# Optimization experiments

Measured on AMD Instinct MI355X. Metric: run time of the kernel, lower is better.

## Reference

```python
import jax, jax.numpy as jnp
import numpy as np

EMBED_DIM = 1024
N1 = 4096
N2 = 4096


def setup_inputs() -> dict:
    key = jax.random.key(0)
    ks = jax.random.split(key, 14)
    s = 1.0 / np.sqrt(EMBED_DIM)
    def lin(k):
        kw, kb = jax.random.split(k)
        W = jax.random.uniform(kw, (EMBED_DIM, EMBED_DIM), jnp.float32, -s, s)
        b = jax.random.uniform(kb, (EMBED_DIM,), jnp.float32, -s, s)
        return W, b
    Wq1, bq1 = lin(ks[0]); Wk1, bk1 = lin(ks[1]); Wv1, bv1 = lin(ks[2])
    Wq2, bq2 = lin(ks[3]); Wk2, bk2 = lin(ks[4]); Wv2, bv2 = lin(ks[5])
    x1 = jax.random.normal(ks[6], (N1, EMBED_DIM), jnp.float32)
    x2 = jax.random.normal(ks[7], (N2, EMBED_DIM), jnp.float32)
    return {
        "input_tensor1": x1, "input_tensor2": x2,
        "Wq1": Wq1, "bq1": bq1, "Wk1": Wk1, "bk1": bk1, "Wv1": Wv1, "bv1": bv1,
        "Wq2": Wq2, "bq2": bq2, "Wk2": Wk2, "bk2": bk2, "Wv2": Wv2, "bv2": bv2,
    }


def reference(input_tensor1, input_tensor2,
              Wq1, bq1, Wk1, bk1, Wv1, bv1,
              Wq2, bq2, Wk2, bk2, Wv2, bv2):
    scale = 1.0 / jnp.sqrt(jnp.asarray(EMBED_DIM, input_tensor1.dtype))
    # torch Linear: y = x @ W.T + b
    q1 = input_tensor1 @ Wq1.T + bq1   # [N1, D]
    k1 = input_tensor1 @ Wk1.T + bk1
    v1 = input_tensor1 @ Wv1.T + bv1
    q2 = input_tensor2 @ Wq2.T + bq2   # [N2, D]
    k2 = input_tensor2 @ Wk2.T + bk2
    v2 = input_tensor2 @ Wv2.T + bv2
    # stream-2 queries attend over stream-1 keys/values
    scores1 = (q2 @ k1.T) * scale                  # [N2, N1]
    probs1 = jax.nn.softmax(scores1, axis=-1)      # dropout p=0 -> identity
    context1 = probs1 @ v1                         # [N2, D]
    # stream-1 queries attend over stream-2 keys/values
    scores2 = (q1 @ k2.T) * scale                  # [N1, N2]
    probs2 = jax.nn.softmax(scores2, axis=-1)
    context2 = probs2 @ v2                         # [N1, D]
    return (context1, context2)
```

## Files before the change

### kernel.cpp

```cpp
#include <hip/hip_runtime.h>
#include <hip/hip_bf16.h>
#include <cstdint>
#include <cstddef>

#define DEVINL __device__ __forceinline__

typedef __attribute__((ext_vector_type(4))) float   f32x4;
typedef __bf16 bf16x8 __attribute__((ext_vector_type(8)));
typedef __attribute__((ext_vector_type(4))) short   short4v;
typedef __attribute__((ext_vector_type(4))) float   float4v;

static constexpr int DIM = 1024;
static constexpr int NTOK = 4096;

DEVINL unsigned short f2bf(float f) {
  unsigned u = __float_as_uint(f);
  u += 0x7FFF + ((u >> 16) & 1);
  return (unsigned short)(u >> 16);
}
DEVINL float bf2f(unsigned short s) {
  return __uint_as_float(((unsigned)s) << 16);
}

DEVINL void gll16(const void* g, void* l) {
  __builtin_amdgcn_global_load_lds(
      (const __attribute__((address_space(1))) void*)g,
      (__attribute__((address_space(3))) void*)l, 16, 0, 0);
}

struct B3 { int bx, by, bz; };
DEVINL B3 xcd_remap(int GX, int GY, int GZ) {
  const int flat = blockIdx.x + GX * (blockIdx.y + GY * blockIdx.z);
  const int nwg  = GX * GY * GZ;
  const int chunk = nwg >> 3;
  const int vbid = (flat & 7) * chunk + (flat >> 3);
  B3 r;
  r.bx = vbid % GX;
  r.by = (vbid / GX) % GY;
  r.bz = vbid / (GX * GY);
  return r;
}

DEVINL void core128(const unsigned short* __restrict__ A, int lda,
                    const unsigned short* __restrict__ B, int ldb,
                    int K, int brow, int bcol, f32x4 acc[4][4])
{
  __shared__ unsigned short lds[32768];
  const int t = threadIdx.x;
  const int w = t >> 6, l = t & 63;
  const int wr = w >> 1, wc = w & 1;
  const int srow = (w << 3) + (l >> 3);
  const int scol = ((l & 7) ^ (l >> 3)) << 3;
  const int l15 = l & 15;
  const int cs0 = (((l >> 4) << 3)        ^ ((l & 7) << 3));
  const int cs1 = ((32 + ((l >> 4) << 3)) ^ ((l & 7) << 3));

  const unsigned short* aL = A + (size_t)(brow * 128 + srow) * lda + scol;
  const unsigned short* bL = B + (size_t)(bcol * 128 + srow) * ldb + scol;

#pragma unroll
  for (int m = 0; m < 4; ++m)
#pragma unroll
    for (int n = 0; n < 4; ++n) {
      f32x4 z = {0.f, 0.f, 0.f, 0.f};
      acc[m][n] = z;
    }

#define STAGE(buf, kt)                                                         \
  _Pragma("unroll")                                                            \
  for (int r = 0; r < 4; ++r) {                                                \
    gll16(aL + (size_t)(r * 32) * lda + (size_t)(kt) * 64,                     \
          lds + (buf) * 16384 + (r * 32 + (w << 3)) * 64);                     \
    gll16(bL + (size_t)(r * 32) * ldb + (size_t)(kt) * 64,                     \
          lds + (buf) * 16384 + 8192 + (r * 32 + (w << 3)) * 64);              \
  }

#define BARR() do { asm volatile("" ::: "memory");                             \
                    __builtin_amdgcn_s_barrier();                              \
                    asm volatile("" ::: "memory"); } while (0)

  const int NT = K >> 6;

  STAGE(0, 0);
  asm volatile("s_waitcnt vmcnt(0)" ::: "memory");
  BARR();

  bf16x8 af[4][2], bfv[4][2];
  for (int kt = 0; kt < NT; ++kt) {
    const int cur = kt & 1;
    if (kt + 1 < NT) STAGE(cur ^ 1, kt + 1);

#pragma unroll
    for (int m = 0; m < 4; ++m) {
      const unsigned short* p = lds + cur * 16384 + (wr * 64 + m * 16 + l15) * 64;
      af[m][0] = *(const bf16x8*)(p + cs0);
      af[m][1] = *(const bf16x8*)(p + cs1);
    }
#pragma unroll
    for (int n = 0; n < 4; ++n) {
      const unsigned short* p = lds + cur * 16384 + 8192 + (wc * 64 + n * 16 + l15) * 64;
      bfv[n][0] = *(const bf16x8*)(p + cs0);
      bfv[n][1] = *(const bf16x8*)(p + cs1);
    }

    __builtin_amdgcn_s_setprio(1);
#pragma unroll
    for (int m = 0; m < 4; ++m)
#pragma unroll
      for (int n = 0; n < 4; ++n) {
        f32x4 c_ = acc[m][n];
        c_ = __builtin_amdgcn_mfma_f32_16x16x32_bf16(af[m][0], bfv[n][0], c_, 0, 0, 0);
        c_ = __builtin_amdgcn_mfma_f32_16x16x32_bf16(af[m][1], bfv[n][1], c_, 0, 0, 0);
        acc[m][n] = c_;
      }
    __builtin_amdgcn_s_setprio(0);

    asm volatile("s_waitcnt vmcnt(0)" ::: "memory");
    BARR();
  }
#undef STAGE
#undef BARR
}

__global__ __launch_bounds__(256, 2)
void gemm128_scores(const unsigned short* __restrict__ A,
                    const unsigned short* __restrict__ B,
                    unsigned short* __restrict__ S, float scale)
{
  const B3 b = xcd_remap(32, 32, 1);
  f32x4 acc[4][4];
  core128(A, DIM, B, DIM, DIM, b.by, b.bx, acc);

  const int t = threadIdx.x, w = t >> 6, l = t & 63;
  const int wr = w >> 1, wc = w & 1;
  const int rr = (l >> 4) * 4, cc = l & 15;
#pragma unroll
  for (int m = 0; m < 4; ++m) {
    const int row0 = b.by * 128 + wr * 64 + m * 16 + rr;
#pragma unroll
    for (int n = 0; n < 4; ++n) {
      const int col = b.bx * 128 + wc * 64 + n * 16 + cc;
#pragma unroll
      for (int i = 0; i < 4; ++i)
        S[(size_t)(row0 + i) * NTOK + col] = f2bf(acc[m][n][i] * scale);
    }
  }
}

__global__ __launch_bounds__(256, 2)
void qkv128(const unsigned short* __restrict__ x1, const unsigned short* __restrict__ x2,
            const unsigned short* __restrict__ W6,
            const float* bq1, const float* bk1, const float* bv1,
            const float* bq2, const float* bk2, const float* bv2,
            unsigned short* q1, unsigned short* k1, unsigned short* v1T,
            unsigned short* q2, unsigned short* k2, unsigned short* v2T)
{
  const B3 b = xcd_remap(8, 32, 6);
  const int g = b.bz;
  const unsigned short* A = (g < 3) ? x1 : x2;
  const unsigned short* W = W6 + (size_t)g * (DIM * DIM);
  const float* bias = (g == 0) ? bq1 : (g == 1) ? bk1 : (g == 2) ? bv1
                    : (g == 3) ? bq2 : (g == 4) ? bk2 : bv2;
  unsigned short* out = (g == 0) ? q1 : (g == 1) ? k1 : (g == 2) ? v1T
                      : (g == 3) ? q2 : (g == 4) ? k2 : v2T;
  const bool vT = (g == 2 || g == 5);

  f32x4 acc[4][4];
  core128(A, DIM, W, DIM, DIM, b.by, b.bx, acc);

  const int t = threadIdx.x, w = t >> 6, l = t & 63;
  const int wr = w >> 1, wc = w & 1;
  const int rr = (l >> 4) * 4, cc = l & 15;

  if (!vT) {
#pragma unroll
    for (int m = 0; m < 4; ++m) {
      const int row0 = b.by * 128 + wr * 64 + m * 16 + rr;
#pragma unroll
      for (int n = 0; n < 4; ++n) {
        const int col = b.bx * 128 + wc * 64 + n * 16 + cc;
        const float bv_ = bias[col];
#pragma unroll
        for (int i = 0; i < 4; ++i)
          out[(size_t)(row0 + i) * DIM + col] = f2bf(acc[m][n][i] + bv_);
      }
    }
  } else {
#pragma unroll
    for (int m = 0; m < 4; ++m) {
      const int row0 = b.by * 128 + wr * 64 + m * 16 + rr;
#pragma unroll
      for (int n = 0; n < 4; ++n) {
        const int col = b.bx * 128 + wc * 64 + n * 16 + cc;
        const float bv_ = bias[col];
        short4v pk;
#pragma unroll
        for (int i = 0; i < 4; ++i) pk[i] = (short)f2bf(acc[m][n][i] + bv_);
        *(short4v*)(out + (size_t)col * NTOK + row0) = pk;
      }
    }
  }
}

__global__ __launch_bounds__(256, 2)
void pv128(const unsigned short* __restrict__ S1,
           const unsigned short* __restrict__ S2,
           const unsigned short* __restrict__ vTcat,
           float* __restrict__ out, float* __restrict__ P)
{
  const B3 b = xcd_remap(16, 32, 2);
  const int bx = b.bx, by = b.by, z = b.bz;
  const unsigned short* A = ((bx < 8) ? S1 : S2) + (size_t)z * 2048;
  const unsigned short* B = vTcat + (size_t)z * 2048;

  f32x4 acc[4][4];
  core128(A, NTOK, B, NTOK, 2048, by, bx, acc);

  const int t = threadIdx.x, w = t >> 6, l = t & 63;
  const int wr = w >> 1, wc = w & 1;
  const int rr = (l >> 4) * 4, cc = l & 15;
#pragma unroll
  for (int m = 0; m < 4; ++m) {
    const int row0 = by * 128 + wr * 64 + m * 16 + rr;
#pragma unroll
    for (int n = 0; n < 4; ++n) {
      const int cg = bx * 128 + wc * 64 + n * 16 + cc;
#pragma unroll
      for (int i = 0; i < 4; ++i) {
        const int r = row0 + i;
        if (z) {
          P[(size_t)r * 2048 + cg] = acc[m][n][i];
        } else {
          float* dst = (cg < 1024) ? (out + (size_t)r * 1024 + cg)
                                   : (out + 4194304 + (size_t)r * 1024 + (cg - 1024));
          *dst = acc[m][n][i];
        }
      }
    }
  }
}

__global__ __launch_bounds__(256)
void add_pv(float* __restrict__ out, const float* __restrict__ P)
{
  const int idx = blockIdx.x * 256 + threadIdx.x;
  const int r  = idx >> 9;
  const int c4 = (idx & 511) << 2;
  const float4v p = *(const float4v*)(P + (size_t)r * 2048 + c4);
  float* dst = (c4 < 1024) ? (out + (size_t)r * 1024 + c4)
                           : (out + 4194304 + (size_t)r * 1024 + (c4 - 1024));
  float4v a = *(const float4v*)dst;
#pragma unroll
  for (int j = 0; j < 4; ++j) a[j] += p[j];
  *(float4v*)dst = a;
}

__global__ __launch_bounds__(256)
void softmax_inplace(unsigned short* __restrict__ S)
{
  const int row = blockIdx.x;
  unsigned short* r = S + (size_t)row * NTOK;
  const int t = threadIdx.x, wave = t >> 6, lane = t & 63;
  __shared__ float red[4];

  bf16x8 d0 = *(const bf16x8*)(r + t * 8);
  bf16x8 d1 = *(const bf16x8*)(r + 2048 + t * 8);
  float v[16];
  {
    const unsigned short* p0 = (const unsigned short*)&d0;
    const unsigned short* p1 = (const unsigned short*)&d1;
#pragma unroll
    for (int j = 0; j < 8; ++j) { v[j] = bf2f(p0[j]); v[8 + j] = bf2f(p1[j]); }
  }
  float mx = v[0];
#pragma unroll
  for (int j = 1; j < 16; ++j) mx = fmaxf(mx, v[j]);
#pragma unroll
  for (int o = 32; o > 0; o >>= 1) mx = fmaxf(mx, __shfl_xor(mx, o));
  if (lane == 0) red[wave] = mx;
  __syncthreads();
  mx = fmaxf(fmaxf(red[0], red[1]), fmaxf(red[2], red[3]));

  float s = 0.f;
#pragma unroll
  for (int j = 0; j < 16; ++j) { v[j] = __expf(v[j] - mx); s += v[j]; }
#pragma unroll
  for (int o = 32; o > 0; o >>= 1) s += __shfl_xor(s, o);
  __syncthreads();
  if (lane == 0) red[wave] = s;
  __syncthreads();
  s = red[0] + red[1] + red[2] + red[3];
  const float inv = 1.0f / s;

  unsigned short o0[8], o1[8];
#pragma unroll
  for (int j = 0; j < 8; ++j) { o0[j] = f2bf(v[j] * inv); o1[j] = f2bf(v[8 + j] * inv); }
  *(bf16x8*)(r + t * 8)        = *(const bf16x8*)o0;
  *(bf16x8*)(r + 2048 + t * 8) = *(const bf16x8*)o1;
}

__global__ __launch_bounds__(256)
void cvt2(const float* __restrict__ a, const float* __restrict__ b,
          unsigned short* __restrict__ oa, unsigned short* __restrict__ ob)
{
  const float* in = blockIdx.y ? b : a;
  unsigned short* out = blockIdx.y ? ob : oa;
  const size_t i = ((size_t)blockIdx.x * 256 + threadIdx.x) * 4;
  float4v x = *(const float4v*)(in + i);
  short4v o;
#pragma unroll
  for (int j = 0; j < 4; ++j) o[j] = (short)f2bf(x[j]);
  *(short4v*)(out + i) = o;
}

__global__ __launch_bounds__(256)
void cvt_w(const float* w0, const float* w1, const float* w2,
           const float* w3, const float* w4, const float* w5,
           unsigned short* __restrict__ W6)
{
  const float* srcs[6] = {w0, w1, w2, w3, w4, w5};
  const float* in = srcs[blockIdx.y];
  unsigned short* out = W6 + (size_t)blockIdx.y * (DIM * DIM);
  const size_t i = ((size_t)blockIdx.x * 256 + threadIdx.x) * 4;
  float4v x = *(const float4v*)(in + i);
  short4v o;
#pragma unroll
  for (int j = 0; j < 4; ++j) o[j] = (short)f2bf(x[j]);
  *(short4v*)(out + i) = o;
}

extern "C" void kernel_launch(void* const* d_in, const int* in_sizes, int n_in,
                              void* d_out, int out_size, void* d_ws, size_t ws_size,
                              hipStream_t stream)
{
  const float* x1  = (const float*)d_in[0];
  const float* x2  = (const float*)d_in[1];
  const float* Wq1 = (const float*)d_in[2];  const float* bq1 = (const float*)d_in[3];
  const float* Wk1 = (const float*)d_in[4];  const float* bk1 = (const float*)d_in[5];
  const float* Wv1 = (const float*)d_in[6];  const float* bv1 = (const float*)d_in[7];
  const float* Wq2 = (const float*)d_in[8];  const float* bq2 = (const float*)d_in[9];
  const float* Wk2 = (const float*)d_in[10]; const float* bk2 = (const float*)d_in[11];
  const float* Wv2 = (const float*)d_in[12]; const float* bv2 = (const float*)d_in[13];
  float* out = (float*)d_out;

  unsigned short* ws  = (unsigned short*)d_ws;
  const size_t NTD = (size_t)NTOK * DIM;
  const size_t SM  = (size_t)NTOK * NTOK;
  unsigned short* x1b = ws;
  unsigned short* x2b = x1b + NTD;
  unsigned short* W6  = x2b + NTD;
  unsigned short* S1  = ws;
  unsigned short* S2  = ws + SM;
  unsigned short* q1  = ws + 2 * SM;
  unsigned short* k1  = q1 + NTD;
  unsigned short* q2  = k1 + NTD;
  unsigned short* k2  = q2 + NTD;
  unsigned short* vT  = k2 + NTD;
  unsigned short* v1T = vT;
  unsigned short* v2T = vT + NTD;
  float* P = (float*)q1;

  const dim3 blk(256);
  cvt2 <<<dim3(NTD / 1024, 2), blk, 0, stream>>>(x1, x2, x1b, x2b);
  cvt_w<<<dim3((DIM * DIM) / 1024, 6), blk, 0, stream>>>(Wq1, Wk1, Wv1, Wq2, Wk2, Wv2, W6);

  qkv128<<<dim3(8, 32, 6), blk, 0, stream>>>(
      x1b, x2b, W6, bq1, bk1, bv1, bq2, bk2, bv2, q1, k1, v1T, q2, k2, v2T);

  const float scale = 0.03125f;

  gemm128_scores<<<dim3(32, 32), blk, 0, stream>>>(q2, k1, S1, scale);
  softmax_inplace<<<dim3(NTOK), blk, 0, stream>>>(S1);
  gemm128_scores<<<dim3(32, 32), blk, 0, stream>>>(q1, k2, S2, scale);
  softmax_inplace<<<dim3(NTOK), blk, 0, stream>>>(S2);

  pv128<<<dim3(16, 32, 2), blk, 0, stream>>>(S1, S2, vT, out, P);
  add_pv<<<dim3(8192), blk, 0, stream>>>(out, P);
}
```

Measured before the change: 263.5 us.

## Halve GEMM K-tile to 32 with new LDS swizzle and raise occupancy

Shrinks the shared GEMM core's K tile from 64 to 32, which halves the LDS footprint and the fragment registers per thread, and rewrites the global-to-LDS load mapping and XOR swizzle for the narrower rows. Launch bounds are raised from 2 to 4 blocks per CU so more workgroups can hide latency. In exchange there are twice as many K iterations, each with a full vmcnt wait and barrier, and less MFMA work per synchronization. The tighter register budget may also cause spills.

```diff
diff --git a/kernel.cpp b/kernel.cpp
--- a/kernel.cpp
+++ b/kernel.cpp
@@ -45,15 +45,14 @@
                     const unsigned short* __restrict__ B, int ldb,
                     int K, int brow, int bcol, f32x4 acc[4][4])
 {
-  __shared__ unsigned short lds[32768];
+  __shared__ unsigned short lds[16384];
   const int t = threadIdx.x;
   const int w = t >> 6, l = t & 63;
   const int wr = w >> 1, wc = w & 1;
-  const int srow = (w << 3) + (l >> 3);
-  const int scol = ((l & 7) ^ (l >> 3)) << 3;
   const int l15 = l & 15;
-  const int cs0 = (((l >> 4) << 3)        ^ ((l & 7) << 3));
-  const int cs1 = ((32 + ((l >> 4) << 3)) ^ ((l & 7) << 3));
+  const int srow = w * 16 + (l >> 2);
+  const int scol = ((l & 3) ^ ((l >> 3) & 3)) << 3;
+  const int cs = (((l >> 4) ^ ((l15 >> 1) & 3)) << 3);
 
   const unsigned short* aL = A + (size_t)(brow * 128 + srow) * lda + scol;
   const unsigned short* bL = B + (size_t)(bcol * 128 + srow) * ldb + scol;
@@ -68,51 +67,41 @@
 
 #define STAGE(buf, kt)                                                         \
   _Pragma("unroll")                                                            \
-  for (int r = 0; r < 4; ++r) {                                                \
-    gll16(aL + (size_t)(r * 32) * lda + (size_t)(kt) * 64,                     \
-          lds + (buf) * 16384 + (r * 32 + (w << 3)) * 64);                     \
-    gll16(bL + (size_t)(r * 32) * ldb + (size_t)(kt) * 64,                     \
-          lds + (buf) * 16384 + 8192 + (r * 32 + (w << 3)) * 64);              \
+  for (int li = 0; li < 2; ++li) {                                             \
+    gll16(aL + (size_t)(li * 64) * lda + (size_t)(kt) * 32,                    \
+          lds + (buf) * 8192 + li * 2048 + w * 512);                           \
+    gll16(bL + (size_t)(li * 64) * ldb + (size_t)(kt) * 32,                    \
+          lds + (buf) * 8192 + 4096 + li * 2048 + w * 512);                    \
   }
 
 #define BARR() do { asm volatile("" ::: "memory");                             \
                     __builtin_amdgcn_s_barrier();                              \
                     asm volatile("" ::: "memory"); } while (0)
 
-  const int NT = K >> 6;
+  const int NT = K >> 5;
 
   STAGE(0, 0);
   asm volatile("s_waitcnt vmcnt(0)" ::: "memory");
   BARR();
 
-  bf16x8 af[4][2], bfv[4][2];
+  bf16x8 af[4], bfv[4];
   for (int kt = 0; kt < NT; ++kt) {
     const int cur = kt & 1;
     if (kt + 1 < NT) STAGE(cur ^ 1, kt + 1);
 
 #pragma unroll
-    for (int m = 0; m < 4; ++m) {
-      const unsigned short* p = lds + cur * 16384 + (wr * 64 + m * 16 + l15) * 64;
-      af[m][0] = *(const bf16x8*)(p + cs0);
-      af[m][1] = *(const bf16x8*)(p + cs1);
-    }
-#pragma unroll
-    for (int n = 0; n < 4; ++n) {
-      const unsigned short* p = lds + cur * 16384 + 8192 + (wc * 64 + n * 16 + l15) * 64;
-      bfv[n][0] = *(const bf16x8*)(p + cs0);
-      bfv[n][1] = *(const bf16x8*)(p + cs1);
-    }
+    for (int m = 0; m < 4; ++m)
+      af[m] = *(const bf16x8*)(lds + cur * 8192 + (wr * 64 + m * 16 + l15) * 32 + cs);
+#pragma unroll
+    for (int n = 0; n < 4; ++n)
+      bfv[n] = *(const bf16x8*)(lds + cur * 8192 + 4096 + (wc * 64 + n * 16 + l15) * 32 + cs);
 
     __builtin_amdgcn_s_setprio(1);
 #pragma unroll
     for (int m = 0; m < 4; ++m)
 #pragma unroll
-      for (int n = 0; n < 4; ++n) {
-        f32x4 c_ = acc[m][n];
-        c_ = __builtin_amdgcn_mfma_f32_16x16x32_bf16(af[m][0], bfv[n][0], c_, 0, 0, 0);
-        c_ = __builtin_amdgcn_mfma_f32_16x16x32_bf16(af[m][1], bfv[n][1], c_, 0, 0, 0);
-        acc[m][n] = c_;
-      }
+      for (int n = 0; n < 4; ++n)
+        acc[m][n] = __builtin_amdgcn_mfma_f32_16x16x32_bf16(af[m], bfv[n], acc[m][n], 0, 0, 0);
     __builtin_amdgcn_s_setprio(0);
 
     asm volatile("s_waitcnt vmcnt(0)" ::: "memory");
@@ -122,7 +111,7 @@
 #undef BARR
 }
 
-__global__ __launch_bounds__(256, 2)
+__global__ __launch_bounds__(256, 4)
 void gemm128_scores(const unsigned short* __restrict__ A,
                     const unsigned short* __restrict__ B,
                     unsigned short* __restrict__ S, float scale)
@@ -147,7 +136,7 @@
   }
 }
 
-__global__ __launch_bounds__(256, 2)
+__global__ __launch_bounds__(256, 4)
 void qkv128(const unsigned short* __restrict__ x1, const unsigned short* __restrict__ x2,
             const unsigned short* __restrict__ W6,
             const float* bq1, const float* bk1, const float* bv1,
@@ -202,7 +191,7 @@
   }
 }
 
-__global__ __launch_bounds__(256, 2)
+__global__ __launch_bounds__(256, 4)
 void pv128(const unsigned short* __restrict__ S1,
            const unsigned short* __restrict__ S2,
            const unsigned short* __restrict__ vTcat,
```

Measured after the change: 297.1 us. 12.8% more time.
